# Kernel optimization log

Measured on AMD Instinct MI355X. Metric: run time of the kernel, lower is better.

Reference implementation:

```python
import jax, jax.numpy as jnp
import numpy as np

GROUP_SIZE = 8
REQUIRED_ZEROS = 4


def _dorefa_quantize(x, bits):
    # tanh-normalize-round
    t = jnp.tanh(x).astype(jnp.float32)
    y = t / jnp.max(jnp.abs(t))
    delta = float(2 ** (bits - 1) - 1)
    _y = jnp.round(y * delta)

    out_c, in_c, h, w = _y.shape
    if in_c < GROUP_SIZE:
        return _y / delta

    g = in_c // GROUP_SIZE
    keep = GROUP_SIZE - REQUIRED_ZEROS  # keep at most 4 non-zeros per group

    # [out_c, g*8, h, w] -> [out_c, g, h, w, 8] (group axis last for top_k)
    yg = _y[:, : g * GROUP_SIZE].reshape(out_c, g, GROUP_SIZE, h, w)
    yg = jnp.transpose(yg, (0, 1, 3, 4, 2))

    # The torch loop zeroes the smallest-|v| non-zeros until >=4 zeros per
    # group. Equivalently: keep only the `keep` largest-|v| entries of each
    # group (zeros have |v|=0, so groups already having >=4 zeros are
    # unchanged). Fully vectorized via batched top-k + one-hot mask.
    absv = jnp.abs(yg)
    _, idx = jax.lax.top_k(absv, keep)                      # [o,g,h,w,keep]
    mask = jax.nn.one_hot(idx, GROUP_SIZE, dtype=yg.dtype).sum(axis=-2)
    yg = yg * mask                                          # [o,g,h,w,8]

    yg = jnp.transpose(yg, (0, 1, 4, 2, 3)).reshape(out_c, g * GROUP_SIZE, h, w)
    out = jnp.concatenate([yg, _y[:, g * GROUP_SIZE :]], axis=1) if g * GROUP_SIZE < in_c else yg
    return out / delta


def setup_inputs() -> dict:
    key = jax.random.key(0)
    x = jax.random.normal(key, (2048, 2048, 3, 3), dtype=jnp.float32)
    return {"x": x, "bits": 8}


def reference(x, bits):
    return _dorefa_quantize(x, bits)
```

## Files before the change

kernel.cpp:

```cpp
#include <hip/hip_runtime.h>
#include <math.h>

#define HW        9
#define GROUP     8
#define KEEP      4
#define DELTA     127.0f
#define INV_DELTA (1.0f / 127.0f)
#define GB_FLOATS 72

#define GB_TILE   32
#define TILE_F    (GB_TILE * GB_FLOATS)
#define TILE_CH   (TILE_F / 256)
#define CELLS     (GB_TILE * HW)
#define WPB       4
#define NT        8

typedef float f32x4 __attribute__((ext_vector_type(4)));

template <int N>
__device__ __forceinline__ void wait_vmcnt() {
    asm volatile("s_waitcnt vmcnt(%0)" :: "n"(N) : "memory");
}

__device__ __forceinline__ unsigned umx(unsigned a, unsigned b) { return a > b ? a : b; }
__device__ __forceinline__ unsigned umn(unsigned a, unsigned b) { return a < b ? a : b; }

__global__ void maxabs_kernel(const float4* __restrict__ x, unsigned* __restrict__ ws, int n4) {
    __shared__ float red[4];
    float m = 0.0f;
    int stride = gridDim.x * blockDim.x;
    #pragma unroll 4
    for (int i = blockIdx.x * blockDim.x + threadIdx.x; i < n4; i += stride) {
        float4 v = x[i];
        m = fmaxf(m, fmaxf(fmaxf(fabsf(v.x), fabsf(v.y)),
                           fmaxf(fabsf(v.z), fabsf(v.w))));
    }
    #pragma unroll
    for (int off = 32; off > 0; off >>= 1)
        m = fmaxf(m, __shfl_down(m, off, 64));
    int wave = threadIdx.x >> 6;
    if ((threadIdx.x & 63) == 0) red[wave] = m;
    __syncthreads();
    if (threadIdx.x == 0) {
        float b = fmaxf(fmaxf(red[0], red[1]), fmaxf(red[2], red[3]));
        atomicMax(ws, __float_as_uint(b));
    }
}

__device__ __attribute__((noinline)) float ref_rz(float xx, float M) {
    float td = (float)tanh((double)xx);
    float y  = td / M;
    return rintf(y * DELTA);
}

__device__ __forceinline__ float fast_tanh(float x) {
    float ax  = fabsf(x);
    float axc = fminf(ax, 10.0f);
    float E   = __expf(2.0f * axc);
    float num = E - 1.0f;
    float den = E + 1.0f;
    float r0  = __builtin_amdgcn_rcpf(den);
    float r   = r0 * fmaf(-den, r0, 2.0f);
    float tl  = copysignf(num * r, x);
    float s = x * x;
    float p = fmaf(s, 0.0035921280f, -0.0088632358f);
    p = fmaf(s, p, 0.021869488f);
    p = fmaf(s, p, -0.053968254f);
    p = fmaf(s, p, 0.13333334f);
    p = fmaf(s, p, -0.33333334f);
    float ts = fmaf(x * s, p, x);
    return (ax <= 0.5f) ? ts : tl;
}

__device__ __forceinline__ void compute_tile(float* ldsw, int lane, float M, float C) {
    #pragma unroll
    for (int c = 0; c < (CELLS + 63) / 64; ++c) {
        int ci = lane + 64 * c;
        if (ci < CELLS) {
            int gb = ci / 9;
            int hw = ci - gb * 9;
            float* cell = ldsw + gb * GB_FLOATS + hw;

            float v8[GROUP];
            unsigned K[GROUP];
            #pragma unroll
            for (int j = 0; j < GROUP; ++j) {
                float xx = cell[9 * j];
                float t  = fast_tanh(xx);
                float z  = t * C;
                float rz = rintf(z);
                float d  = 0.5f - fabsf(z - rz);
                if (d < fmaf(2e-6f, fabsf(z), 5e-7f))
                    rz = ref_rz(xx, M);
                v8[j] = rz;
                K[j] = ((unsigned)fabsf(rz) << 3) | (unsigned)(7 - j);
            }

            unsigned s0 = K[0], s1 = K[1], s2 = K[2], s3 = K[3];
            unsigned s4 = K[4], s5 = K[5], s6 = K[6], s7 = K[7];
            #define CE_(x, y) { unsigned _h = umx(x, y), _l = umn(x, y); x = _h; y = _l; }
            CE_(s0, s1) CE_(s2, s3) CE_(s0, s2) CE_(s1, s3) CE_(s1, s2)
            CE_(s4, s5) CE_(s6, s7) CE_(s4, s6) CE_(s5, s7) CE_(s5, s6)
            #undef CE_
            unsigned T = umx(umx(umn(s0, s6), umn(s1, s5)),
                             umx(umn(s2, s4), umx(s3, s7)));

            #pragma unroll
            for (int j = 0; j < GROUP; ++j)
                cell[9 * j] = (K[j] >= T) ? (v8[j] * INV_DELTA) : 0.0f;
        }
    }
}

__global__ __launch_bounds__(256, 2) void quant_kernel(const float* __restrict__ x,
                             float* __restrict__ out,
                             const unsigned* __restrict__ ws,
                             int n_gb) {
    __shared__ float lds[WPB][2][TILE_F];
    __shared__ float sM, sC;
    if (threadIdx.x == 0) {
        float mm = (float)tanh((double)__uint_as_float(*ws));
        sM = mm;
        sC = (float)(127.0 / (double)mm);
    }
    __syncthreads();
    float M = sM, C = sC;

    const int wv   = threadIdx.x >> 6;
    const int lane = threadIdx.x & 63;
    const int wave_id = blockIdx.x * WPB + wv;

    const size_t tbase0 = (size_t)wave_id * NT * TILE_F;

    #pragma unroll
    for (int b = 0; b < 2; ++b) {
        const float* src = x + tbase0 + (size_t)b * TILE_F;
        float* ldsw = &lds[wv][b][0];
        #pragma unroll
        for (int k = 0; k < TILE_CH; ++k) {
            __builtin_amdgcn_global_load_lds(
                (__attribute__((address_space(1))) void*)(src + k * 256 + lane * 4),
                (__attribute__((address_space(3))) void*)(ldsw + k * 256),
                16, 0, 0);
        }
    }

    #pragma unroll
    for (int i = 0; i < NT; ++i) {
        if (i == 0)            wait_vmcnt<9>();
        else if (i == 1)       wait_vmcnt<18>();
        else if (i == NT - 1)  wait_vmcnt<18>();
        else                   wait_vmcnt<27>();
        __builtin_amdgcn_sched_barrier(0);

        float* ldsw = &lds[wv][i & 1][0];
        compute_tile(ldsw, lane, M, C);

        f32x4 sv[TILE_CH];
        const f32x4* l4 = (const f32x4*)ldsw;
        #pragma unroll
        for (int k = 0; k < TILE_CH; ++k) sv[k] = l4[k * 64 + lane];
        asm volatile("s_waitcnt lgkmcnt(0)" ::: "memory");
        __builtin_amdgcn_sched_barrier(0);

        if (i + 2 < NT) {
            const float* src = x + tbase0 + (size_t)(i + 2) * TILE_F;
            #pragma unroll
            for (int k = 0; k < TILE_CH; ++k) {
                __builtin_amdgcn_global_load_lds(
                    (__attribute__((address_space(1))) void*)(src + k * 256 + lane * 4),
                    (__attribute__((address_space(3))) void*)(ldsw + k * 256),
                    16, 0, 0);
            }
        }

        f32x4* dst4 = (f32x4*)(out + tbase0 + (size_t)i * TILE_F);
        #pragma unroll
        for (int k = 0; k < TILE_CH; ++k)
            dst4[k * 64 + lane] = sv[k];
    }
}

extern "C" void kernel_launch(void* const* d_in, const int* in_sizes, int n_in,
                              void* d_out, int out_size, void* d_ws, size_t ws_size,
                              hipStream_t stream) {
    const float* x = (const float*)d_in[0];
    float* out = (float*)d_out;
    unsigned* ws = (unsigned*)d_ws;

    int n = in_sizes[0];
    int n4 = n / 4;
    int n_gb = n / GB_FLOATS;

    hipMemsetAsync(ws, 0, sizeof(unsigned), stream);

    maxabs_kernel<<<2048, 256, 0, stream>>>((const float4*)x, ws, n4);

    int blocks_q = n_gb / (GB_TILE * NT * WPB);
    quant_kernel<<<blocks_q, 256, 0, stream>>>(x, out, ws, n_gb);
}
```

Before: 325.0 us.

## Replace async LDS double-buffer with register prefetch and single LDS tile

Drops the global_load_lds double-buffered pipeline in favour of loading the next tile into registers, then writing it to a single per-wave LDS buffer before compute. Halving LDS use and raising launch bounds to 3 blocks per SM is meant to raise occupancy, and NT is cut to 4 tiles per wave so more blocks are launched. The cost is extra VGPRs for the two register buffers, an explicit register-to-LDS copy, and a shallower prefetch distance (one tile instead of two).

```diff
diff --git a/kernel.cpp b/kernel.cpp
--- a/kernel.cpp
+++ b/kernel.cpp
@@ -13,14 +13,9 @@
 #define TILE_CH   (TILE_F / 256)
 #define CELLS     (GB_TILE * HW)
 #define WPB       4
-#define NT        8
+#define NT        4
 
 typedef float f32x4 __attribute__((ext_vector_type(4)));
-
-template <int N>
-__device__ __forceinline__ void wait_vmcnt() {
-    asm volatile("s_waitcnt vmcnt(%0)" :: "n"(N) : "memory");
-}
 
 __device__ __forceinline__ unsigned umx(unsigned a, unsigned b) { return a > b ? a : b; }
 __device__ __forceinline__ unsigned umn(unsigned a, unsigned b) { return a < b ? a : b; }
@@ -112,11 +107,11 @@
     }
 }
 
-__global__ __launch_bounds__(256, 2) void quant_kernel(const float* __restrict__ x,
+__global__ __launch_bounds__(256, 3) void quant_kernel(const float* __restrict__ x,
                              float* __restrict__ out,
                              const unsigned* __restrict__ ws,
                              int n_gb) {
-    __shared__ float lds[WPB][2][TILE_F];
+    __shared__ float lds[WPB][TILE_F];
     __shared__ float sM, sC;
     if (threadIdx.x == 0) {
         float mm = (float)tanh((double)__uint_as_float(*ws));
@@ -131,53 +126,41 @@
     const int wave_id = blockIdx.x * WPB + wv;
 
     const size_t tbase0 = (size_t)wave_id * NT * TILE_F;
+    float* ldsw = &lds[wv][0];
+    f32x4* l4 = (f32x4*)ldsw;
 
-    #pragma unroll
-    for (int b = 0; b < 2; ++b) {
-        const float* src = x + tbase0 + (size_t)b * TILE_F;
-        float* ldsw = &lds[wv][b][0];
+    f32x4 ra[TILE_CH], rb[TILE_CH];
+
+    {
+        const f32x4* s4 = (const f32x4*)(x + tbase0);
         #pragma unroll
-        for (int k = 0; k < TILE_CH; ++k) {
-            __builtin_amdgcn_global_load_lds(
-                (__attribute__((address_space(1))) void*)(src + k * 256 + lane * 4),
-                (__attribute__((address_space(3))) void*)(ldsw + k * 256),
-                16, 0, 0);
-        }
+        for (int k = 0; k < TILE_CH; ++k) ra[k] = s4[k * 64 + lane];
     }
 
     #pragma unroll
     for (int i = 0; i < NT; ++i) {
-        if (i == 0)            wait_vmcnt<9>();
-        else if (i == 1)       wait_vmcnt<18>();
-        else if (i == NT - 1)  wait_vmcnt<18>();
-        else                   wait_vmcnt<27>();
+        f32x4* cur = (i & 1) ? rb : ra;
+        f32x4* nxt = (i & 1) ? ra : rb;
+
+        if (i + 1 < NT) {
+            const f32x4* sn = (const f32x4*)(x + tbase0 + (size_t)(i + 1) * TILE_F);
+            #pragma unroll
+            for (int k = 0; k < TILE_CH; ++k) nxt[k] = sn[k * 64 + lane];
+        }
         __builtin_amdgcn_sched_barrier(0);
 
-        float* ldsw = &lds[wv][i & 1][0];
-        compute_tile(ldsw, lane, M, C);
-
-        f32x4 sv[TILE_CH];
-        const f32x4* l4 = (const f32x4*)ldsw;
         #pragma unroll
-        for (int k = 0; k < TILE_CH; ++k) sv[k] = l4[k * 64 + lane];
-        asm volatile("s_waitcnt lgkmcnt(0)" ::: "memory");
+        for (int k = 0; k < TILE_CH; ++k) l4[k * 64 + lane] = cur[k];
         __builtin_amdgcn_sched_barrier(0);
 
-        if (i + 2 < NT) {
-            const float* src = x + tbase0 + (size_t)(i + 2) * TILE_F;
-            #pragma unroll
-            for (int k = 0; k < TILE_CH; ++k) {
-                __builtin_amdgcn_global_load_lds(
-                    (__attribute__((address_space(1))) void*)(src + k * 256 + lane * 4),
-                    (__attribute__((address_space(3))) void*)(ldsw + k * 256),
-                    16, 0, 0);
-            }
-        }
+        compute_tile(ldsw, lane, M, C);
+        __builtin_amdgcn_sched_barrier(0);
 
         f32x4* dst4 = (f32x4*)(out + tbase0 + (size_t)i * TILE_F);
         #pragma unroll
         for (int k = 0; k < TILE_CH; ++k)
-            dst4[k * 64 + lane] = sv[k];
+            dst4[k * 64 + lane] = l4[k * 64 + lane];
+        __builtin_amdgcn_sched_barrier(0);
     }
 }
 
```

After: 305.6 us. 6.0% less time.
